# Kernel optimization log

Hardware: AMD Instinct MI355X
Metric: run time of the kernel (lower is better)

Reference implementation:

```python
import jax, jax.numpy as jnp
import numpy as np

LN_EPS = 1e-5      # torch nn.LayerNorm default
NORM_EPS = 1e-12   # torch F.normalize default


def _layer_norm(x, gamma, beta):
    mu = jnp.mean(x, axis=-1, keepdims=True)
    var = jnp.mean((x - mu) ** 2, axis=-1, keepdims=True)
    return (x - mu) * jax.lax.rsqrt(var + LN_EPS) * gamma + beta


def _l2_normalize_rows(w):
    n = jnp.sqrt(jnp.sum(w * w, axis=1, keepdims=True))
    return w / jnp.maximum(n, NORM_EPS)


def setup_inputs() -> dict:
    key = jax.random.key(0)
    B, D = 32768, 512
    ks = jax.random.split(key, 4)
    return {
        "stimulus": jax.random.normal(ks[0], (B, D), dtype=jnp.float32),
        "prev_activation": jax.random.normal(ks[1], (B, D), dtype=jnp.float32),
        "W": jax.random.normal(ks[2], (D, D), dtype=jnp.float32),
        "Wr": jax.random.normal(ks[3], (D, D), dtype=jnp.float32),
        "alpha": jnp.full((D,), 0.1, dtype=jnp.float32),
        "decay": jnp.full((D,), 0.01, dtype=jnp.float32),
        "ln_act_gamma": jnp.ones((D,), dtype=jnp.float32),
        "ln_act_beta": jnp.zeros((D,), dtype=jnp.float32),
        "ln_rec_gamma": jnp.ones((D,), dtype=jnp.float32),
        "ln_rec_beta": jnp.zeros((D,), dtype=jnp.float32),
    }


def reference(stimulus, prev_activation, W, Wr, alpha, decay,
              ln_act_gamma, ln_act_beta, ln_rec_gamma, ln_rec_beta):
    # recurrent path
    rec_out = prev_activation @ Wr                      # [B, D]
    rec_norm = _layer_norm(rec_out, ln_rec_gamma, ln_rec_beta)
    # stimulus path
    stim_out = stimulus @ W                             # [B, D]
    final = jax.nn.relu(stim_out + rec_norm)
    final = _layer_norm(final, ln_act_gamma, ln_act_beta)

    # Hebbian weight update (detached in the original module)
    heb_upd = jnp.einsum('bi,bj->ij', stimulus, stim_out) * alpha[None, :]
    rec_upd = jnp.einsum('bi,bj->ij', prev_activation, rec_out) * alpha[None, :]
    # diag(decay) @ W is a row-wise broadcast scale
    new_W = _l2_normalize_rows(W + heb_upd - decay[:, None] * W)
    new_Wr = _l2_normalize_rows(Wr + rec_upd - decay[:, None] * Wr)

    return final, new_W, new_Wr
```

## Files before the change

kernel.cpp:

```cpp
#include <hip/hip_runtime.h>
#include <stdint.h>

typedef unsigned int u32;
typedef unsigned short u16;
typedef float  f32x4 __attribute__((ext_vector_type(4)));
typedef u32    u32x4 __attribute__((ext_vector_type(4)));
typedef __bf16 bf16x8 __attribute__((ext_vector_type(8)));

static __device__ __forceinline__ u16 f2bf(float f){
  u32 u = __builtin_bit_cast(u32, f);
  return (u16)((u + 0x7FFFu + ((u >> 16) & 1u)) >> 16);
}

static __device__ __forceinline__ void async16(const void* g, void* l){
  __builtin_amdgcn_global_load_lds((const __attribute__((address_space(1))) u32*)g,
                                   (__attribute__((address_space(3))) u32*)l, 16, 0, 0);
}

static __device__ __forceinline__ float wave_sum(float v){
#pragma unroll
  for (int o = 32; o > 0; o >>= 1) v += __shfl_xor(v, o, 64);
  return v;
}

__global__ __launch_bounds__(256) void k_cvt2(const float* __restrict__ s0, const float* __restrict__ s1,
                                              u16* __restrict__ dn0, u16* __restrict__ dn1,
                                              u16* __restrict__ dt0, u16* __restrict__ dt1,
                                              int wn, int wt){
  const float* __restrict__ src = blockIdx.z ? s1 : s0;
  u16* __restrict__ dn = blockIdx.z ? dn1 : dn0;
  u16* __restrict__ dt = blockIdx.z ? dt1 : dt0;
  __shared__ u16 lt[64*72];
  const int c0 = blockIdx.x * 64;
  const int r0 = blockIdx.y * 64;
  const int tid = threadIdx.x;
  const int rr = tid >> 4, c4 = tid & 15;
#pragma unroll
  for (int p = 0; p < 4; ++p){
    int r = rr + p*16;
    f32x4 f = *(const f32x4*)(src + (size_t)(r0 + r)*512 + c0 + c4*4);
    u16 b0 = f2bf(f[0]), b1 = f2bf(f[1]), b2 = f2bf(f[2]), b3 = f2bf(f[3]);
    if (wt){
      lt[(c4*4 + 0)*72 + r] = b0;
      lt[(c4*4 + 1)*72 + r] = b1;
      lt[(c4*4 + 2)*72 + r] = b2;
      lt[(c4*4 + 3)*72 + r] = b3;
    }
    if (wn){
      u32* qp = (u32*)(dn + (size_t)(r0 + r)*512 + c0 + c4*4);
      qp[0] = (u32)b0 | ((u32)b1 << 16);
      qp[1] = (u32)b2 | ((u32)b3 << 16);
    }
  }
  if (!wt) return;
  __syncthreads();
  const int c = tid >> 2, bg = tid & 3;
  const u32x4* lp = (const u32x4*)(lt + c*72 + bg*16);
  u32x4 w0 = lp[0], w1 = lp[1];
  u16* drow = dt + (size_t)(c0 + c)*32768 + r0 + bg*16;
  *(u32x4*)drow = w0;
  *(u32x4*)(drow + 8) = w1;
}

__global__ __launch_bounds__(256) void k_tpose(const u16* __restrict__ s0, const u16* __restrict__ s1,
                                               u16* __restrict__ d0, u16* __restrict__ d1){
  const u16* __restrict__ src = blockIdx.z ? s1 : s0;
  u16* __restrict__ dst = blockIdx.z ? d1 : d0;
  __shared__ u16 lt[64*72];
  const int c0 = blockIdx.x * 64, r0 = blockIdx.y * 64;
  const int tid = threadIdx.x;
  const int rr = tid >> 3, c8 = tid & 7;
#pragma unroll
  for (int p = 0; p < 2; ++p){
    int r = rr + p*32;
    u32x4 w = *(const u32x4*)(src + (size_t)(r0 + r)*512 + c0 + c8*8);
#pragma unroll
    for (int e = 0; e < 4; ++e){
      u32 v = w[e];
      lt[(c8*8 + 2*e    )*72 + r] = (u16)(v & 0xFFFFu);
      lt[(c8*8 + 2*e + 1)*72 + r] = (u16)(v >> 16);
    }
  }
  __syncthreads();
  const int c = tid >> 2, bg = tid & 3;
  const u32x4* lp = (const u32x4*)(lt + c*72 + bg*16);
  u32x4 w0 = lp[0], w1 = lp[1];
  u16* drow = dst + (size_t)(c0 + c)*32768 + r0 + bg*16;
  *(u32x4*)drow = w0;
  *(u32x4*)(drow + 8) = w1;
}

__global__ __launch_bounds__(256) void k_tcvt(const float* __restrict__ s0, const float* __restrict__ s1,
                                              u16* __restrict__ d0, u16* __restrict__ d1,
                                              int R, int C){
  const float* __restrict__ src = blockIdx.z ? s1 : s0;
  u16* __restrict__ dst = blockIdx.z ? d1 : d0;
  __shared__ u16 lt[64*72];
  const int c0 = blockIdx.x * 64, r0 = blockIdx.y * 64;
  const int tid = threadIdx.x;
  const int rr = tid >> 4, c4 = tid & 15;
#pragma unroll
  for (int p = 0; p < 4; ++p){
    int r = rr + p*16;
    f32x4 f = *(const f32x4*)(src + (size_t)(r0 + r)*C + c0 + c4*4);
#pragma unroll
    for (int e = 0; e < 4; ++e) lt[(c4*4 + e)*72 + r] = f2bf(f[e]);
  }
  __syncthreads();
  const int c = tid >> 2, bg = tid & 3;
  const u32x4* lp = (const u32x4*)(lt + c*72 + bg*16);
  u32x4 w0 = lp[0], w1 = lp[1];
  u16* drow = dst + (size_t)(c0 + c)*R + r0 + bg*16;
  *(u32x4*)drow = w0;
  *(u32x4*)(drow + 8) = w1;
}

__global__ __launch_bounds__(512) void k_gemm_fwd(const u16* __restrict__ SN, const u16* __restrict__ PN,
                                                  const u16* __restrict__ Wt, const u16* __restrict__ Wrt,
                                                  u16* __restrict__ SO, u16* __restrict__ RO,
                                                  u16* __restrict__ SOT, u16* __restrict__ ROT){
  __shared__ char smem[67584];
  u16* sA = (u16*)smem;
  u16* sB = (u16*)(smem + 32768);
  const int tid = threadIdx.x;
  const int lane = tid & 63, wid = tid >> 6;
  const int wm = wid >> 1, wn = wid & 1;
  const int l15 = lane & 15, q = lane >> 4;
  const int id = blockIdx.x;
  const int c8 = id & 7, g = id >> 3;
  const int sel = g >> 6, h = g & 63;
  const int yb = c8*16 + (h >> 2), xb = h & 3;
  const int m0 = yb * 256, n0 = xb * 128;
  const u16* __restrict__ A  = sel ? PN  : SN;
  const u16* __restrict__ Bt = sel ? Wrt : Wt;
  u16* __restrict__ Cn = sel ? RO  : SO;
  u16* __restrict__ Ct = sel ? ROT : SOT;

  f32x4 acc[4][4];
  const f32x4 vzero = {0.f, 0.f, 0.f, 0.f};
#pragma unroll
  for (int a = 0; a < 4; ++a)
#pragma unroll
    for (int b = 0; b < 4; ++b) acc[a][b] = vzero;

#pragma unroll 1
  for (int kt = 0; kt < 8; ++kt){
    const int k0 = kt*64;
#pragma unroll
    for (int it = 0; it < 4; ++it){
      int gg0 = it*512 + tid;
      int r = gg0 >> 3, gp = gg0 & 7, gsw = gp ^ (r & 7);
      async16(A + (size_t)(m0 + r)*512 + k0 + gsw*8, (char*)sA + (size_t)gg0*16);
    }
#pragma unroll
    for (int it = 0; it < 2; ++it){
      int gg0 = it*512 + tid;
      int r = gg0 >> 3, gp = gg0 & 7, gsw = gp ^ (r & 7);
      async16(Bt + (size_t)(n0 + r)*512 + k0 + gsw*8, (char*)sB + (size_t)gg0*16);
    }
    __syncthreads();
#pragma unroll
    for (int kk = 0; kk < 2; ++kk){
      bf16x8 af[4], bfv[4];
#pragma unroll
      for (int mt = 0; mt < 4; ++mt){
        int r = wm*64 + mt*16 + l15;
        int gsw = (kk*4 + q) ^ (r & 7);
        af[mt] = *(const bf16x8*)(sA + (size_t)(r*8 + gsw)*8);
      }
#pragma unroll
      for (int nt = 0; nt < 4; ++nt){
        int r = wn*64 + nt*16 + l15;
        int gsw = (kk*4 + q) ^ (r & 7);
        bfv[nt] = *(const bf16x8*)(sB + (size_t)(r*8 + gsw)*8);
      }
#pragma unroll
      for (int mt = 0; mt < 4; ++mt)
#pragma unroll
        for (int nt = 0; nt < 4; ++nt)
          acc[mt][nt] = __builtin_amdgcn_mfma_f32_16x16x32_bf16(af[mt], bfv[nt], acc[mt][nt], 0, 0, 0);
    }
    __syncthreads();
  }

  u16* lt = (u16*)smem;
#pragma unroll
  for (int mt = 0; mt < 4; ++mt)
#pragma unroll
    for (int nt = 0; nt < 4; ++nt){
      f32x4 v = acc[mt][nt];
      u16 b0 = f2bf(v[0]), b1 = f2bf(v[1]), b2 = f2bf(v[2]), b3 = f2bf(v[3]);
      int n = wn*64 + nt*16 + l15;
      int mb = wm*64 + mt*16 + q*4;
      u16* cn = Cn + (size_t)(m0 + mb)*512 + n0 + n;
      cn[0] = b0; cn[512] = b1; cn[1024] = b2; cn[1536] = b3;
      *(u32*)(lt + n*264 + mb)     = (u32)b0 | ((u32)b1 << 16);
      *(u32*)(lt + n*264 + mb + 2) = (u32)b2 | ((u32)b3 << 16);
    }
  __syncthreads();
#pragma unroll
  for (int p = 0; p < 8; ++p){
    int gg0 = p*512 + tid;
    int n = gg0 >> 5, mg = gg0 & 31;
    u32x4 w = *(const u32x4*)(lt + n*264 + mg*8);
    *(u32x4*)(Ct + (size_t)(n0 + n)*32768 + m0 + mg*8) = w;
  }
}

__global__ __launch_bounds__(512) void k_gemm_upd(const u16* __restrict__ A0, const u16* __restrict__ B0,
                                                  const u16* __restrict__ A1, const u16* __restrict__ B1,
                                                  float* __restrict__ part){
  __shared__ char smem[49152];
  u16* sA = (u16*)smem;
  u16* sB = (u16*)(smem + 16384);
  const int tid = threadIdx.x;
  const int lane = tid & 63, wid = tid >> 6;
  const int wm = wid >> 2, wn = wid & 3;
  const int l15 = lane & 15, q = lane >> 4;
  const int id = blockIdx.x;
  const int c8 = id & 7, g = id >> 3;
  const int zz = c8*8 + (g >> 3);
  const int xy = g & 7;
  const int mat = zz >> 5, sp = zz & 31;
  const int yb = xy & 3, xb = xy >> 2;
  const u16* __restrict__ A = mat ? A1 : A0;
  const u16* __restrict__ B = mat ? B1 : B0;
  const int m0 = yb * 128, n0 = xb * 256;
  const int kb = sp * 1024;

  f32x4 acc[4][4];
  const f32x4 vzero = {0.f, 0.f, 0.f, 0.f};
#pragma unroll
  for (int a = 0; a < 4; ++a)
#pragma unroll
    for (int b = 0; b < 4; ++b) acc[a][b] = vzero;

#pragma unroll 1
  for (int kt = 0; kt < 16; ++kt){
    const int k0 = kb + kt*64;
#pragma unroll
    for (int it = 0; it < 2; ++it){
      int gg0 = it*512 + tid;
      int r = gg0 >> 3, gp = gg0 & 7, gsw = gp ^ (r & 7);
      async16(A + (size_t)(m0 + r)*32768 + k0 + gsw*8, (char*)sA + (size_t)gg0*16);
    }
#pragma unroll
    for (int it = 0; it < 4; ++it){
      int gg0 = it*512 + tid;
      int r = gg0 >> 3, gp = gg0 & 7, gsw = gp ^ (r & 7);
      async16(B + (size_t)(n0 + r)*32768 + k0 + gsw*8, (char*)sB + (size_t)gg0*16);
    }
    __syncthreads();
#pragma unroll
    for (int kk = 0; kk < 2; ++kk){
      bf16x8 af[4], bfv[4];
#pragma unroll
      for (int mt = 0; mt < 4; ++mt){
        int r = wm*64 + mt*16 + l15;
        int gsw = (kk*4 + q) ^ (r & 7);
        af[mt] = *(const bf16x8*)(sA + (size_t)(r*8 + gsw)*8);
      }
#pragma unroll
      for (int nt = 0; nt < 4; ++nt){
        int r = wn*64 + nt*16 + l15;
        int gsw = (kk*4 + q) ^ (r & 7);
        bfv[nt] = *(const bf16x8*)(sB + (size_t)(r*8 + gsw)*8);
      }
#pragma unroll
      for (int mt = 0; mt < 4; ++mt)
#pragma unroll
        for (int nt = 0; nt < 4; ++nt)
          acc[mt][nt] = __builtin_amdgcn_mfma_f32_16x16x32_bf16(af[mt], bfv[nt], acc[mt][nt], 0, 0, 0);
    }
    __syncthreads();
  }

  float* dst = part + (size_t)(mat*32 + sp)*262144;
#pragma unroll
  for (int mt = 0; mt < 4; ++mt)
#pragma unroll
    for (int nt = 0; nt < 4; ++nt){
      f32x4 v = acc[mt][nt];
      int n = wn*64 + nt*16 + l15;
      int mb = wm*64 + mt*16 + q*4;
      float* d = dst + (size_t)(m0 + mb)*512 + n0 + n;
      d[0] = v[0]; d[512] = v[1]; d[1024] = v[2]; d[1536] = v[3];
    }
}

__global__ __launch_bounds__(256) void k_ln(const u16* __restrict__ SO, const u16* __restrict__ RO,
                                            const float* __restrict__ ga, const float* __restrict__ ba,
                                            const float* __restrict__ gr, const float* __restrict__ br,
                                            float* __restrict__ out){
  const int wid = threadIdx.x >> 6, lane = threadIdx.x & 63;
  const size_t b = (size_t)blockIdx.x*4 + wid;
  const int c = lane*8;
  float x[8], t[8];
  {
    u32x4 u = *(const u32x4*)(RO + b*512 + c);
#pragma unroll
    for (int i = 0; i < 4; ++i){
      u32 w = u[i];
      x[2*i]   = __uint_as_float(w << 16);
      x[2*i+1] = __uint_as_float(w & 0xFFFF0000u);
    }
  }
  float s = 0.f, ss = 0.f;
#pragma unroll
  for (int e = 0; e < 8; ++e){ s += x[e]; ss += x[e]*x[e]; }
  s = wave_sum(s); ss = wave_sum(ss);
  float mu = s*(1.f/512.f);
  float var = fmaxf(ss*(1.f/512.f) - mu*mu, 0.f);
  float rs = rsqrtf(var + 1e-5f);
  f32x4 g0 = *(const f32x4*)(gr + c), g1 = *(const f32x4*)(gr + c + 4);
  f32x4 h0 = *(const f32x4*)(br + c), h1 = *(const f32x4*)(br + c + 4);
  {
    u32x4 u = *(const u32x4*)(SO + b*512 + c);
    float so[8];
#pragma unroll
    for (int i = 0; i < 4; ++i){
      u32 w = u[i];
      so[2*i]   = __uint_as_float(w << 16);
      so[2*i+1] = __uint_as_float(w & 0xFFFF0000u);
    }
#pragma unroll
    for (int e = 0; e < 4; ++e) t[e]   = fmaxf(so[e]   + (x[e]  -mu)*rs*g0[e] + h0[e], 0.f);
#pragma unroll
    for (int e = 0; e < 4; ++e) t[4+e] = fmaxf(so[4+e] + (x[4+e]-mu)*rs*g1[e] + h1[e], 0.f);
  }
  float s2 = 0.f, ss2 = 0.f;
#pragma unroll
  for (int e = 0; e < 8; ++e){ s2 += t[e]; ss2 += t[e]*t[e]; }
  s2 = wave_sum(s2); ss2 = wave_sum(ss2);
  float mu2 = s2*(1.f/512.f);
  float var2 = fmaxf(ss2*(1.f/512.f) - mu2*mu2, 0.f);
  float rs2 = rsqrtf(var2 + 1e-5f);
  f32x4 G0 = *(const f32x4*)(ga + c), G1 = *(const f32x4*)(ga + c + 4);
  f32x4 H0 = *(const f32x4*)(ba + c), H1 = *(const f32x4*)(ba + c + 4);
  f32x4 o0, o1;
#pragma unroll
  for (int e = 0; e < 4; ++e){
    o0[e] = (t[e]   - mu2)*rs2*G0[e] + H0[e];
    o1[e] = (t[4+e] - mu2)*rs2*G1[e] + H1[e];
  }
  *(f32x4*)(out + b*512 + c)     = o0;
  *(f32x4*)(out + b*512 + c + 4) = o1;
}

__global__ __launch_bounds__(256) void k_finalize(const float* __restrict__ W0, const float* __restrict__ W1,
                                                  const float* __restrict__ part,
                                                  const float* __restrict__ alpha, const float* __restrict__ decay,
                                                  float* __restrict__ out){
  const int i = blockIdx.x, mat = blockIdx.y;
  const int t = threadIdx.x;
  const float* Wm = mat ? W1 : W0;
  const float* pb = part + (size_t)mat*32*262144 + (size_t)i*512;
  const float dc = decay[i];
  float v[2], ssq = 0.f;
#pragma unroll
  for (int h = 0; h < 2; ++h){
    int j = t + h*256;
    float acc = 0.f;
#pragma unroll
    for (int sp = 0; sp < 32; ++sp) acc += pb[(size_t)sp*262144 + j];
    float val = Wm[(size_t)i*512 + j]*(1.f - dc) + alpha[j]*acc;
    v[h] = val; ssq += val*val;
  }
  float wsum = wave_sum(ssq);
  __shared__ float red[4];
  const int lane = t & 63, wid = t >> 6;
  if (lane == 0) red[wid] = wsum;
  __syncthreads();
  float tot = red[0] + red[1] + red[2] + red[3];
  float rn = 1.f / fmaxf(sqrtf(tot), 1e-12f);
  out[(size_t)mat*262144 + (size_t)i*512 + t]       = v[0]*rn;
  out[(size_t)mat*262144 + (size_t)i*512 + t + 256] = v[1]*rn;
}

extern "C" void kernel_launch(void* const* d_in, const int* in_sizes, int n_in,
                              void* d_out, int out_size, void* d_ws, size_t ws_size,
                              hipStream_t stream) {
  const float* S  = (const float*)d_in[0];
  const float* P  = (const float*)d_in[1];
  const float* W  = (const float*)d_in[2];
  const float* Wr = (const float*)d_in[3];
  const float* alpha = (const float*)d_in[4];
  const float* decay = (const float*)d_in[5];
  const float* ga = (const float*)d_in[6];
  const float* ba = (const float*)d_in[7];
  const float* gr = (const float*)d_in[8];
  const float* br = (const float*)d_in[9];
  float* out = (float*)d_out;

  char* ws = (char*)d_ws;
  const size_t M32 = 33554432;
  const bool big = ws_size >= (size_t)269484032;

  u16 *SN, *PN, *ST, *PT, *SOT, *ROT, *SO, *RO, *Wt, *Wrt;
  if (big){
    SN  = (u16*)(ws);
    PN  = (u16*)(ws + 1*M32);
    ST  = (u16*)(ws + 2*M32);
    PT  = (u16*)(ws + 3*M32);
    SOT = (u16*)(ws + 4*M32);
    ROT = (u16*)(ws + 5*M32);
    SO  = (u16*)(ws + 6*M32);
    RO  = (u16*)(ws + 7*M32);
    Wt  = (u16*)(ws + 8*M32);
    Wrt = (u16*)(ws + 8*M32 + 524288);
  } else {
    SN  = (u16*)(ws);
    PN  = (u16*)(ws + 1*M32);
    SOT = (u16*)(ws + 2*M32);
    ROT = (u16*)(ws + 3*M32);
    SO  = (u16*)(ws + 4*M32);
    RO  = (u16*)(ws + 5*M32);
    Wt  = (u16*)(ws + 6*M32);
    Wrt = (u16*)(ws + 6*M32 + 524288);
    ST  = SO;
    PT  = RO;
  }
  float* part = (float*)ws;

  k_cvt2<<<dim3(8, 512, 2), dim3(256), 0, stream>>>(S, P, SN, PN, ST, PT, 1, big ? 1 : 0);
  k_tcvt<<<dim3(8, 8, 2), dim3(256), 0, stream>>>(W, Wr, Wt, Wrt, 512, 512);
  k_gemm_fwd<<<dim3(1024), dim3(512), 0, stream>>>(SN, PN, Wt, Wrt, SO, RO, SOT, ROT);
  k_ln<<<dim3(8192), dim3(256), 0, stream>>>(SO, RO, ga, ba, gr, br, out);
  if (!big)
    k_tpose<<<dim3(8, 512, 2), dim3(256), 0, stream>>>(SN, PN, ST, PT);
  k_gemm_upd<<<dim3(512), dim3(512), 0, stream>>>(ST, SOT, PT, ROT, part);
  k_finalize<<<dim3(512, 2), dim3(256), 0, stream>>>(W, Wr, part, alpha, decay, out + 16777216);
}
```

Baseline: 347.7 us.

## Split fp32-to-bf16 conversion from transpose and use wider swizzled transpose tiles

Replaces the fused convert+transpose kernel with a plain vectorized fp32-to-bf16 conversion kernel plus a separate bf16 transpose kernel. The new transpose handles 256-row by 64-column tiles, packs pairs of rows into 32-bit words and uses an XOR-swizzled LDS layout, so it writes 16-byte chunks and avoids the 16-bit scattered LDS stores of the old kernel. In the big-workspace path this adds an extra pass that re-reads the bf16 data for the transpose, which costs bandwidth in exchange for more efficient individual kernels.

```diff
diff --git a/kernel.cpp b/kernel.cpp
--- a/kernel.cpp
+++ b/kernel.cpp
@@ -23,71 +23,63 @@
   return v;
 }
 
-__global__ __launch_bounds__(256) void k_cvt2(const float* __restrict__ s0, const float* __restrict__ s1,
-                                              u16* __restrict__ dn0, u16* __restrict__ dn1,
-                                              u16* __restrict__ dt0, u16* __restrict__ dt1,
-                                              int wn, int wt){
-  const float* __restrict__ src = blockIdx.z ? s1 : s0;
-  u16* __restrict__ dn = blockIdx.z ? dn1 : dn0;
-  u16* __restrict__ dt = blockIdx.z ? dt1 : dt0;
-  __shared__ u16 lt[64*72];
-  const int c0 = blockIdx.x * 64;
-  const int r0 = blockIdx.y * 64;
-  const int tid = threadIdx.x;
-  const int rr = tid >> 4, c4 = tid & 15;
-#pragma unroll
-  for (int p = 0; p < 4; ++p){
-    int r = rr + p*16;
-    f32x4 f = *(const f32x4*)(src + (size_t)(r0 + r)*512 + c0 + c4*4);
-    u16 b0 = f2bf(f[0]), b1 = f2bf(f[1]), b2 = f2bf(f[2]), b3 = f2bf(f[3]);
-    if (wt){
-      lt[(c4*4 + 0)*72 + r] = b0;
-      lt[(c4*4 + 1)*72 + r] = b1;
-      lt[(c4*4 + 2)*72 + r] = b2;
-      lt[(c4*4 + 3)*72 + r] = b3;
-    }
-    if (wn){
-      u32* qp = (u32*)(dn + (size_t)(r0 + r)*512 + c0 + c4*4);
-      qp[0] = (u32)b0 | ((u32)b1 << 16);
-      qp[1] = (u32)b2 | ((u32)b3 << 16);
-    }
-  }
-  if (!wt) return;
-  __syncthreads();
-  const int c = tid >> 2, bg = tid & 3;
-  const u32x4* lp = (const u32x4*)(lt + c*72 + bg*16);
-  u32x4 w0 = lp[0], w1 = lp[1];
-  u16* drow = dt + (size_t)(c0 + c)*32768 + r0 + bg*16;
-  *(u32x4*)drow = w0;
-  *(u32x4*)(drow + 8) = w1;
-}
-
-__global__ __launch_bounds__(256) void k_tpose(const u16* __restrict__ s0, const u16* __restrict__ s1,
-                                               u16* __restrict__ d0, u16* __restrict__ d1){
+__global__ __launch_bounds__(256) void k_cvt(const float* __restrict__ s0, const float* __restrict__ s1,
+                                             u16* __restrict__ d0, u16* __restrict__ d1){
+  const float* __restrict__ src = blockIdx.y ? s1 : s0;
+  u16* __restrict__ dst = blockIdx.y ? d1 : d0;
+  size_t i = ((size_t)blockIdx.x*256 + threadIdx.x) * 8;
+  f32x4 a = *(const f32x4*)(src + i);
+  f32x4 b = *(const f32x4*)(src + i + 4);
+  u32x4 w;
+  w[0] = (u32)f2bf(a[0]) | ((u32)f2bf(a[1]) << 16);
+  w[1] = (u32)f2bf(a[2]) | ((u32)f2bf(a[3]) << 16);
+  w[2] = (u32)f2bf(b[0]) | ((u32)f2bf(b[1]) << 16);
+  w[3] = (u32)f2bf(b[2]) | ((u32)f2bf(b[3]) << 16);
+  *(u32x4*)(dst + i) = w;
+}
+
+__global__ __launch_bounds__(256) void k_tp(const u16* __restrict__ s0, const u16* __restrict__ s1,
+                                            u16* __restrict__ d0, u16* __restrict__ d1){
   const u16* __restrict__ src = blockIdx.z ? s1 : s0;
   u16* __restrict__ dst = blockIdx.z ? d1 : d0;
-  __shared__ u16 lt[64*72];
-  const int c0 = blockIdx.x * 64, r0 = blockIdx.y * 64;
-  const int tid = threadIdx.x;
-  const int rr = tid >> 3, c8 = tid & 7;
-#pragma unroll
-  for (int p = 0; p < 2; ++p){
-    int r = rr + p*32;
-    u32x4 w = *(const u32x4*)(src + (size_t)(r0 + r)*512 + c0 + c8*8);
+  __shared__ u32 st[64*128];
+  const int r0 = blockIdx.x * 256;
+  const int c0 = blockIdx.y * 64;
+  const int t = threadIdx.x;
+  const int tb = t & 127, th = t >> 7;
+  const u16* pA = src + (size_t)(r0 + 2*tb)*512 + c0 + th*32;
+  u32 a[16], b[16];
+  {
+    u32x4 a0 = *(const u32x4*)pA,        a1 = *(const u32x4*)(pA + 8);
+    u32x4 a2 = *(const u32x4*)(pA + 16), a3 = *(const u32x4*)(pA + 24);
+    u32x4 b0 = *(const u32x4*)(pA + 512),  b1 = *(const u32x4*)(pA + 520);
+    u32x4 b2 = *(const u32x4*)(pA + 528),  b3 = *(const u32x4*)(pA + 536);
 #pragma unroll
     for (int e = 0; e < 4; ++e){
-      u32 v = w[e];
-      lt[(c8*8 + 2*e    )*72 + r] = (u16)(v & 0xFFFFu);
-      lt[(c8*8 + 2*e + 1)*72 + r] = (u16)(v >> 16);
-    }
+      a[e] = a0[e]; a[4+e] = a1[e]; a[8+e] = a2[e]; a[12+e] = a3[e];
+      b[e] = b0[e]; b[4+e] = b1[e]; b[8+e] = b2[e]; b[12+e] = b3[e];
+    }
+  }
+  const int g5 = tb >> 2, w2 = tb & 3;
+#pragma unroll
+  for (int m = 0; m < 16; ++m){
+    u32 lo = a[m], hi = b[m];
+    u32 w0 = (lo & 0xFFFFu) | (hi << 16);
+    u32 w1 = (lo >> 16) | (hi & 0xFFFF0000u);
+    int d0i = th*32 + 2*m, d1i = d0i + 1;
+    st[d0i*128 + ((g5 ^ (d0i & 7)) << 2) + w2] = w0;
+    st[d1i*128 + ((g5 ^ (d1i & 7)) << 2) + w2] = w1;
   }
   __syncthreads();
-  const int c = tid >> 2, bg = tid & 3;
-  const u32x4* lp = (const u32x4*)(lt + c*72 + bg*16);
-  u32x4 w0 = lp[0], w1 = lp[1];
-  u16* drow = dst + (size_t)(c0 + c)*32768 + r0 + bg*16;
-  *(u32x4*)drow = w0;
-  *(u32x4*)(drow + 8) = w1;
+  const int rd = t >> 2, rg = t & 3;
+  u16* drow = dst + (size_t)(c0 + rd)*32768 + r0;
+#pragma unroll
+  for (int k = 0; k < 8; ++k){
+    int gp = rg + 4*k;
+    int slot = gp ^ (rd & 7);
+    u32x4 w = *(const u32x4*)(st + rd*128 + slot*4);
+    *(u32x4*)(drow + rg*8 + 32*k) = w;
+  }
 }
 
 __global__ __launch_bounds__(256) void k_tcvt(const float* __restrict__ s0, const float* __restrict__ s1,
@@ -422,12 +414,14 @@
   }
   float* part = (float*)ws;
 
-  k_cvt2<<<dim3(8, 512, 2), dim3(256), 0, stream>>>(S, P, SN, PN, ST, PT, 1, big ? 1 : 0);
+  k_cvt<<<dim3(8192, 2), dim3(256), 0, stream>>>(S, P, SN, PN);
+  if (big)
+    k_tp<<<dim3(128, 8, 2), dim3(256), 0, stream>>>(SN, PN, ST, PT);
   k_tcvt<<<dim3(8, 8, 2), dim3(256), 0, stream>>>(W, Wr, Wt, Wrt, 512, 512);
   k_gemm_fwd<<<dim3(1024), dim3(512), 0, stream>>>(SN, PN, Wt, Wrt, SO, RO, SOT, ROT);
   k_ln<<<dim3(8192), dim3(256), 0, stream>>>(SO, RO, ga, ba, gr, br, out);
   if (!big)
-    k_tpose<<<dim3(8, 512, 2), dim3(256), 0, stream>>>(SN, PN, ST, PT);
+    k_tp<<<dim3(128, 8, 2), dim3(256), 0, stream>>>(SN, PN, ST, PT);
   k_gemm_upd<<<dim3(512), dim3(512), 0, stream>>>(ST, SOT, PT, ROT, part);
   k_finalize<<<dim3(512, 2), dim3(256), 0, stream>>>(W, Wr, part, alpha, decay, out + 16777216);
 }
```

After: 346.1 us. Within noise of the previous version (-0.4%).
